# Kernel optimization log

Measured on AMD Instinct MI355X. Metric: run time of the kernel, lower is better.

Reference implementation:

```python
import jax, jax.numpy as jnp
import numpy as np


def _mhc_kernels():
    # Malvar-He-Cutler 5x5 interpolation kernels, shape (4, 1, 5, 5) OIHW
    G_at_RB = np.array([[0, 0, -1, 0, 0], [0, 0, 2, 0, 0], [-1, 2, 4, 2, -1],
                        [0, 0, 2, 0, 0], [0, 0, -1, 0, 0]], dtype=np.float32) / 8
    R_at_G_Rrow = np.array([[0, 0, 0.5, 0, 0], [0, -1, 0, -1, 0], [-1, 4, 5, 4, -1],
                            [0, -1, 0, -1, 0], [0, 0, 0.5, 0, 0]], dtype=np.float32) / 8
    R_at_G_Brow = np.array([[0, 0, -1, 0, 0], [0, -1, 4, -1, 0], [0.5, 0, 5, 0, 0.5],
                            [0, -1, 4, -1, 0], [0, 0, -1, 0, 0]], dtype=np.float32) / 8
    R_at_B = np.array([[0, 0, -1.5, 0, 0], [0, 2, 0, 2, 0], [-1.5, 0, 6, 0, -1.5],
                       [0, 2, 0, 2, 0], [0, 0, -1.5, 0, 0]], dtype=np.float32) / 8
    return np.stack([G_at_RB, R_at_G_Rrow, R_at_G_Brow, R_at_B], axis=0)[:, None, :, :]


def setup_inputs() -> dict:
    key = jax.random.key(0)
    H, W = 4096, 6144  # 24 MP raw frame
    x = jax.random.randint(key, (H, W), 0, 16777216, dtype=jnp.int32)
    kernels = jnp.asarray(_mhc_kernels())  # fixed buffer values, (4,1,5,5)
    return {"x": x, "kernels": kernels}


def reference(x, kernels):
    xf = x.astype(jnp.float32)  # [H, W]
    # reflect pad by 2 and convolve with the 4 MHC kernels in one conv
    xp = jnp.pad(xf, 2, mode="reflect")[None, None]  # [1,1,H+4,W+4]
    res = jax.lax.conv_general_dilated(
        xp, kernels, window_strides=(1, 1), padding="VALID",
        dimension_numbers=("NCHW", "OIHW", "NCHW"))[0]  # [4, H, W]
    Gi, Rgr, Rgb, Rb = res[0], res[1], res[2], res[3]

    z = jnp.zeros_like(xf)
    # RGGB mosaic: R at (even,even), G at (even,odd)+(odd,even), B at (odd,odd)
    R = (z.at[::2, ::2].set(xf[::2, ::2])
           .at[::2, 1::2].set(Rgr[::2, 1::2])
           .at[1::2, ::2].set(Rgb[1::2, ::2])
           .at[1::2, 1::2].set(Rb[1::2, 1::2]))
    G = (z.at[::2, 1::2].set(xf[::2, 1::2])
           .at[1::2, ::2].set(xf[1::2, ::2])
           .at[::2, ::2].set(Gi[::2, ::2])
           .at[1::2, 1::2].set(Gi[1::2, 1::2]))
    B = (z.at[1::2, 1::2].set(xf[1::2, 1::2])
           .at[1::2, ::2].set(Rgr[1::2, ::2])
           .at[::2, 1::2].set(Rgb[::2, 1::2])
           .at[::2, ::2].set(Rb[::2, ::2]))

    rgb = jnp.stack([R, G, B], axis=-1)  # [H, W, 3]
    return jnp.clip(rgb, 0, 16777215).astype(jnp.int32)
```

## Files before the change

### kernel.cpp

```cpp
#include <hip/hip_runtime.h>

#define IMG_H 4096
#define IMG_W 6144

constexpr int TILE_W = 128;
constexpr int TILE_H = 16;
constexpr int PITCH  = TILE_W + 4;
constexpr int LROWS  = TILE_H + 4;

__device__ __forceinline__ float convG(const float* p) {
    return ( -p[-2*PITCH] + 2.f*p[-PITCH] + 2.f*p[PITCH] - p[2*PITCH]
             - p[-2] + 2.f*p[-1] + 4.f*p[0] + 2.f*p[1] - p[2] ) * 0.125f;
}
__device__ __forceinline__ float convRrow(const float* p) {
    return ( 0.5f*(p[-2*PITCH] + p[2*PITCH])
             - (p[-PITCH-1] + p[-PITCH+1] + p[PITCH-1] + p[PITCH+1])
             - (p[-2] + p[2]) + 4.f*(p[-1] + p[1]) + 5.f*p[0] ) * 0.125f;
}
__device__ __forceinline__ float convBrow(const float* p) {
    return ( -(p[-2*PITCH] + p[2*PITCH])
             - (p[-PITCH-1] + p[-PITCH+1] + p[PITCH-1] + p[PITCH+1])
             + 4.f*(p[-PITCH] + p[PITCH]) + 0.5f*(p[-2] + p[2]) + 5.f*p[0] ) * 0.125f;
}
__device__ __forceinline__ float convRB(const float* p) {
    return ( -1.5f*(p[-2*PITCH] + p[2*PITCH] + p[-2] + p[2])
             + 2.f*(p[-PITCH-1] + p[-PITCH+1] + p[PITCH-1] + p[PITCH+1])
             + 6.f*p[0] ) * 0.125f;
}

__device__ __forceinline__ int clampi(float v) {
    v = fminf(fmaxf(v, 0.f), 16777215.f);
    return (int)v;
}

__global__ __launch_bounds__(256)
void demosaic_kernel(const int* __restrict__ x, int* __restrict__ out) {
    __shared__ float s[LROWS][PITCH];

    const int gx0 = blockIdx.x * TILE_W;
    const int gy0 = blockIdx.y * TILE_H;
    const int tid = threadIdx.x;

    for (int idx = tid; idx < LROWS * PITCH; idx += 256) {
        int r = idx / PITCH;
        int c = idx - r * PITCH;
        int gr = gy0 + r - 2;
        gr = gr < 0 ? -gr : (gr >= IMG_H ? 2 * IMG_H - 2 - gr : gr);
        int gc = gx0 + c - 2;
        gc = gc < 0 ? -gc : (gc >= IMG_W ? 2 * IMG_W - 2 - gc : gc);
        s[r][c] = (float)x[gr * IMG_W + gc];
    }
    __syncthreads();

    const int lane = tid & 63;
    const int ty   = tid >> 6;
    const int c    = 2 * lane;

    #pragma unroll
    for (int k = 0; k < 4; ++k) {
        const int r  = ty + 4 * k;
        const int gi = gy0 + r;
        const float* pe = &s[r + 2][c + 2];
        const float* po = pe + 1;

        const float xe = pe[0];
        const float xo = po[0];

        int Re, Ge, Be, Ro, Go, Bo;
        if ((r & 1) == 0) {
            Re = clampi(xe);
            Ge = clampi(convG(pe));
            Be = clampi(convRB(pe));
            Ro = clampi(convRrow(po));
            Go = clampi(xo);
            Bo = clampi(convBrow(po));
        } else {
            Re = clampi(convBrow(pe));
            Ge = clampi(xe);
            Be = clampi(convRrow(pe));
            Ro = clampi(convRB(po));
            Go = clampi(convG(po));
            Bo = clampi(xo);
        }

        long base = ((long)gi * IMG_W + (gx0 + c)) * 3;
        int2* o2 = (int2*)(out + base);
        o2[0] = make_int2(Re, Ge);
        o2[1] = make_int2(Be, Ro);
        o2[2] = make_int2(Go, Bo);
    }
}

extern "C" void kernel_launch(void* const* d_in, const int* in_sizes, int n_in,
                              void* d_out, int out_size, void* d_ws, size_t ws_size,
                              hipStream_t stream) {
    const int* x = (const int*)d_in[0];
    int* out = (int*)d_out;
    dim3 grid(IMG_W / TILE_W, IMG_H / TILE_H);
    demosaic_kernel<<<grid, 256, 0, stream>>>(x, out);
}
```

Before: 394.9 us.

## Vectorize tile loads and stage outputs in LDS for coalesced nontemporal stores

```diff
diff --git a/kernel.cpp b/kernel.cpp
--- a/kernel.cpp
+++ b/kernel.cpp
@@ -5,89 +5,118 @@
 
 constexpr int TILE_W = 128;
 constexpr int TILE_H = 16;
-constexpr int PITCH  = TILE_W + 4;
-constexpr int LROWS  = TILE_H + 4;
+constexpr int LPAD   = 4;
+constexpr int PITCH  = 136;
+constexpr int LROWS  = 20;
 
-__device__ __forceinline__ float convG(const float* p) {
-    return ( -p[-2*PITCH] + 2.f*p[-PITCH] + 2.f*p[PITCH] - p[2*PITCH]
-             - p[-2] + 2.f*p[-1] + 4.f*p[0] + 2.f*p[1] - p[2] ) * 0.125f;
+typedef int i4 __attribute__((ext_vector_type(4)));
+
+__device__ __forceinline__ int reflect_h(int r) {
+    return r < 0 ? -r : (r >= IMG_H ? 2 * IMG_H - 2 - r : r);
 }
-__device__ __forceinline__ float convRrow(const float* p) {
-    return ( 0.5f*(p[-2*PITCH] + p[2*PITCH])
-             - (p[-PITCH-1] + p[-PITCH+1] + p[PITCH-1] + p[PITCH+1])
-             - (p[-2] + p[2]) + 4.f*(p[-1] + p[1]) + 5.f*p[0] ) * 0.125f;
+__device__ __forceinline__ int reflect_w(int c) {
+    return c < 0 ? -c : (c >= IMG_W ? 2 * IMG_W - 2 - c : c);
 }
-__device__ __forceinline__ float convBrow(const float* p) {
-    return ( -(p[-2*PITCH] + p[2*PITCH])
-             - (p[-PITCH-1] + p[-PITCH+1] + p[PITCH-1] + p[PITCH+1])
-             + 4.f*(p[-PITCH] + p[PITCH]) + 0.5f*(p[-2] + p[2]) + 5.f*p[0] ) * 0.125f;
-}
-__device__ __forceinline__ float convRB(const float* p) {
-    return ( -1.5f*(p[-2*PITCH] + p[2*PITCH] + p[-2] + p[2])
-             + 2.f*(p[-PITCH-1] + p[-PITCH+1] + p[PITCH-1] + p[PITCH+1])
-             + 6.f*p[0] ) * 0.125f;
-}
-
 __device__ __forceinline__ int clampi(float v) {
-    v = fminf(fmaxf(v, 0.f), 16777215.f);
-    return (int)v;
+    return (int)fminf(fmaxf(v, 0.f), 16777215.f);
 }
 
 __global__ __launch_bounds__(256)
 void demosaic_kernel(const int* __restrict__ x, int* __restrict__ out) {
-    __shared__ float s[LROWS][PITCH];
+    __shared__ __align__(16) char smem[24576];
+    float (*sin_)[PITCH] = (float (*)[PITCH])smem;
+    int* sout = (int*)smem;
 
+    const int tid = threadIdx.x;
     const int gx0 = blockIdx.x * TILE_W;
     const int gy0 = blockIdx.y * TILE_H;
-    const int tid = threadIdx.x;
 
-    for (int idx = tid; idx < LROWS * PITCH; idx += 256) {
-        int r = idx / PITCH;
-        int c = idx - r * PITCH;
-        int gr = gy0 + r - 2;
-        gr = gr < 0 ? -gr : (gr >= IMG_H ? 2 * IMG_H - 2 - gr : gr);
-        int gc = gx0 + c - 2;
-        gc = gc < 0 ? -gc : (gc >= IMG_W ? 2 * IMG_W - 2 - gc : gc);
-        s[r][c] = (float)x[gr * IMG_W + gc];
+    #pragma unroll
+    for (int it = 0; it < 3; ++it) {
+        int idx = tid + it * 256;
+        if (idx < LROWS * 32) {
+            int r = idx >> 5, v = idx & 31;
+            int gr = reflect_h(gy0 + r - 2);
+            i4 q = *(const i4*)(x + (long)gr * IMG_W + gx0 + 4 * v);
+            float4 f = make_float4((float)q.x, (float)q.y, (float)q.z, (float)q.w);
+            *(float4*)&sin_[r][LPAD + 4 * v] = f;
+        }
+    }
+    if (tid < 80) {
+        int r = tid >> 2, h = tid & 3;
+        int gr = reflect_h(gy0 + r - 2);
+        int lc = (h < 2) ? (2 + h) : (130 + h);
+        int gc = reflect_w(gx0 + lc - LPAD);
+        sin_[r][lc] = (float)x[(long)gr * IMG_W + gc];
     }
     __syncthreads();
 
-    const int lane = tid & 63;
-    const int ty   = tid >> 6;
-    const int c    = 2 * lane;
+    const int p  = tid & 63;
+    const int ty = tid >> 6;
+    const int cl = LPAD + 2 * p;
+
+    int rr[4][6];
 
     #pragma unroll
     for (int k = 0; k < 4; ++k) {
-        const int r  = ty + 4 * k;
-        const int gi = gy0 + r;
-        const float* pe = &s[r + 2][c + 2];
-        const float* po = pe + 1;
+        const int r = ty + 4 * k;
+        float w[5][6];
+        #pragma unroll
+        for (int i = 0; i < 5; ++i) {
+            float2 a  = *(const float2*)&sin_[r + i][cl - 2];
+            float2 b  = *(const float2*)&sin_[r + i][cl];
+            float2 c2 = *(const float2*)&sin_[r + i][cl + 2];
+            w[i][0] = a.x;  w[i][1] = a.y;
+            w[i][2] = b.x;  w[i][3] = b.y;
+            w[i][4] = c2.x; w[i][5] = c2.y;
+        }
+        const float xe = w[2][2], xo = w[2][3];
 
-        const float xe = pe[0];
-        const float xo = po[0];
+        if ((ty & 1) == 0) {
+            float Ge = (-w[0][2] + 2.f*(w[1][2]+w[3][2]) + 4.f*w[2][2] - w[4][2]
+                        - w[2][0] + 2.f*(w[2][1]+w[2][3]) - w[2][4]) * 0.125f;
+            float Ce = (-1.5f*(w[0][2]+w[4][2]+w[2][0]+w[2][4])
+                        + 2.f*(w[1][1]+w[1][3]+w[3][1]+w[3][3]) + 6.f*w[2][2]) * 0.125f;
+            float RRo = (0.5f*(w[0][3]+w[4][3]) - (w[1][2]+w[1][4]+w[3][2]+w[3][4])
+                         - (w[2][1]+w[2][5]) + 4.f*(w[2][2]+w[2][4]) + 5.f*w[2][3]) * 0.125f;
+            float RBo = (-(w[0][3]+w[4][3]) - (w[1][2]+w[1][4]+w[3][2]+w[3][4])
+                         + 4.f*(w[1][3]+w[3][3]) + 0.5f*(w[2][1]+w[2][5]) + 5.f*w[2][3]) * 0.125f;
+            rr[k][0] = clampi(xe);  rr[k][1] = clampi(Ge);  rr[k][2] = clampi(Ce);
+            rr[k][3] = clampi(RRo); rr[k][4] = clampi(xo);  rr[k][5] = clampi(RBo);
+        } else {
+            float RBe = (-(w[0][2]+w[4][2]) - (w[1][1]+w[1][3]+w[3][1]+w[3][3])
+                         + 4.f*(w[1][2]+w[3][2]) + 0.5f*(w[2][0]+w[2][4]) + 5.f*w[2][2]) * 0.125f;
+            float RRe = (0.5f*(w[0][2]+w[4][2]) - (w[1][1]+w[1][3]+w[3][1]+w[3][3])
+                         - (w[2][0]+w[2][4]) + 4.f*(w[2][1]+w[2][3]) + 5.f*w[2][2]) * 0.125f;
+            float Co  = (-1.5f*(w[0][3]+w[4][3]+w[2][1]+w[2][5])
+                         + 2.f*(w[1][2]+w[1][4]+w[3][2]+w[3][4]) + 6.f*w[2][3]) * 0.125f;
+            float Go  = (-w[0][3] + 2.f*(w[1][3]+w[3][3]) + 4.f*w[2][3] - w[4][3]
+                         - w[2][1] + 2.f*(w[2][2]+w[2][4]) - w[2][5]) * 0.125f;
+            rr[k][0] = clampi(RBe); rr[k][1] = clampi(xe);  rr[k][2] = clampi(RRe);
+            rr[k][3] = clampi(Co);  rr[k][4] = clampi(Go);  rr[k][5] = clampi(xo);
+        }
+    }
 
-        int Re, Ge, Be, Ro, Go, Bo;
-        if ((r & 1) == 0) {
-            Re = clampi(xe);
-            Ge = clampi(convG(pe));
-            Be = clampi(convRB(pe));
-            Ro = clampi(convRrow(po));
-            Go = clampi(xo);
-            Bo = clampi(convBrow(po));
-        } else {
-            Re = clampi(convBrow(pe));
-            Ge = clampi(xe);
-            Be = clampi(convRrow(pe));
-            Ro = clampi(convRB(po));
-            Go = clampi(convG(po));
-            Bo = clampi(xo);
-        }
+    __syncthreads();
 
-        long base = ((long)gi * IMG_W + (gx0 + c)) * 3;
-        int2* o2 = (int2*)(out + base);
-        o2[0] = make_int2(Re, Ge);
-        o2[1] = make_int2(Be, Ro);
-        o2[2] = make_int2(Go, Bo);
+    #pragma unroll
+    for (int k = 0; k < 4; ++k) {
+        int r = ty + 4 * k;
+        int2* o = (int2*)&sout[r * (TILE_W * 3) + 6 * p];
+        o[0] = make_int2(rr[k][0], rr[k][1]);
+        o[1] = make_int2(rr[k][2], rr[k][3]);
+        o[2] = make_int2(rr[k][4], rr[k][5]);
+    }
+    __syncthreads();
+
+    #pragma unroll
+    for (int it = 0; it < 6; ++it) {
+        int j = tid + it * 256;
+        i4 q = *(const i4*)&sout[4 * j];
+        int r  = j / 96;
+        int wv = j - r * 96;
+        int* dst = out + (long)(gy0 + r) * (IMG_W * 3) + gx0 * 3 + 4 * wv;
+        __builtin_nontemporal_store(q, (i4*)dst);
     }
 }
 
```

Measured after the change: 360.2 us. 8.8% less time.
